# Kernel optimization log

Hardware: AMD Instinct MI355X
Metric: run time of the kernel (lower is better)

The kernel has to match this reference:

```python
import jax, jax.numpy as jnp
import numpy as np

B, C, IC, W, H, Z = 2, 128, 64, 32, 32, 128  # sub_sample=True -> new_z = Z//2
BN_EPS = 1e-5


def setup_inputs() -> dict:
    key = jax.random.key(0)
    ks = jax.random.split(key, 14)
    n = lambda k, shape, sc=1.0: jax.random.normal(k, shape, jnp.float32) * sc
    return {
        "x": n(ks[0], (B, C, W, H, Z)),
        "g_w": n(ks[1], (IC, C), 0.05), "g_b": n(ks[2], (IC,), 0.05),
        "theta_w": n(ks[3], (IC, C), 0.05), "theta_b": n(ks[4], (IC,), 0.05),
        "phi_w": n(ks[5], (IC, C), 0.05), "phi_b": n(ks[6], (IC,), 0.05),
        "cat_w": n(ks[7], (2 * IC,), 0.1),           # Conv2d(2*IC -> 1, 1x1, bias=False)
        "W_w": n(ks[8], (C, IC), 0.05), "W_b": n(ks[9], (C,), 0.05),
        "bn_g": n(ks[10], (C,), 0.1), "bn_b": n(ks[11], (C,), 0.1),
        "bn_m": n(ks[12], (C,), 0.1),
        "bn_v": jax.random.uniform(ks[13], (C,), jnp.float32, 0.5, 1.5),
    }


def _conv1x1(x, w, b):
    # 1x1x1 Conv3d == per-voxel channel matmul. x: (b,c,w,h,z), w: (o,c)
    y = jnp.einsum('bcwhz,oc->bowhz', x, w)
    return y + b[None, :, None, None, None]


def _pool_z(t):
    # MaxPool3d(kernel=(1,1,2)): halve last dim by pairwise max
    return t.reshape(*t.shape[:-1], t.shape[-1] // 2, 2).max(-1)


def reference(x, g_w, g_b, theta_w, theta_b, phi_w, phi_b, cat_w,
              W_w, W_b, bn_g, bn_b, bn_m, bn_v):
    b, c, w, h, z = x.shape
    ic = g_w.shape[0]
    nz = z // 2  # sub_sample

    g_x = _pool_z(_conv1x1(x, g_w, g_b))                     # (b, ic, w, h, nz)
    g_x = g_x.transpose(0, 2, 3, 4, 1).reshape(-1, nz, ic)    # (n, nz, ic), n=b*w*h

    theta = _conv1x1(x, theta_w, theta_b)                     # (b, ic, w, h, z)
    theta = theta.transpose(0, 2, 3, 1, 4).reshape(-1, ic, z)  # (n, ic, z)
    phi = _pool_z(_conv1x1(x, phi_w, phi_b))                  # (b, ic, w, h, nz)
    phi = phi.transpose(0, 2, 3, 1, 4).reshape(-1, ic, nz)     # (n, ic, nz)

    # concat + 1x1 Conv2d(2ic->1) + ReLU == relu(w_t . theta_i + w_p . phi_j)
    a = jnp.einsum('nci,c->ni', theta, cat_w[:ic])             # (n, z)
    bb = jnp.einsum('ncj,c->nj', phi, cat_w[ic:])              # (n, nz)
    f = jax.nn.relu(a[:, :, None] + bb[:, None, :]) / nz       # (n, z, nz), /N norm

    y = jnp.einsum('nij,njc->nic', f, g_x)                     # (n, z, ic)
    y = y.reshape(b, w, h, z, ic).transpose(0, 4, 1, 2, 3)      # (b, ic, w, h, z)

    Wy = _conv1x1(y, W_w, W_b)                                 # (b, c, w, h, z)
    scale = (bn_g / jnp.sqrt(bn_v + BN_EPS))[None, :, None, None, None]
    Wy = (Wy - bn_m[None, :, None, None, None]) * scale + bn_b[None, :, None, None, None]
    return Wy + x
```

## Files before the change

### kernel.cpp

```cpp
#include <hip/hip_runtime.h>
#include <hip/hip_bf16.h>


#define C_      128
#define IC_     64
#define Z_      128
#define NZ_     64
#define CSTRIDE 131072
#define NPIX    2048

typedef __attribute__((ext_vector_type(8))) short short8;
typedef __attribute__((ext_vector_type(4))) float f32x4;

union S8 { short8 s; uint4 u4; unsigned short h[8]; };

__device__ __forceinline__ unsigned short f2b(float f) {
    union { __hip_bfloat16 h; unsigned short u; } cv;
    cv.h = __float2bfloat16(f);
    return cv.u;
}
__device__ __forceinline__ float b2f(unsigned short u) {
    union { float f; unsigned int i; } cv; cv.i = ((unsigned int)u) << 16; return cv.f;
}

__global__ void nlb_prep(
    const float* __restrict__ g_w,   const float* __restrict__ theta_w,
    const float* __restrict__ phi_w, const float* __restrict__ W_w,
    const float* __restrict__ g_b,   const float* __restrict__ theta_b,
    const float* __restrict__ phi_b, const float* __restrict__ cat_w,
    const float* __restrict__ W_b,   const float* __restrict__ bn_g,
    const float* __restrict__ bn_b,  const float* __restrict__ bn_m,
    const float* __restrict__ bn_v,
    unsigned short* __restrict__ wcat, unsigned short* __restrict__ Wwb,
    float* __restrict__ twp, float* __restrict__ alphap, float* __restrict__ betap,
    float* __restrict__ cbp, float* __restrict__ cw2p, float* __restrict__ tbp)
{
    const int t = threadIdx.x;
    for (int idx = t; idx < 128 * 128; idx += 256) {
        const int oc = idx >> 7, c = idx & 127;
        const float v = (oc < 64) ? g_w[oc * 128 + c] : phi_w[(oc - 64) * 128 + c];
        wcat[idx] = f2b(v);
    }
    for (int idx = t; idx < 128 * 64; idx += 256)
        Wwb[idx] = f2b(W_w[idx]);
    if (t < 128) {
        float s = 0.f;
        for (int oc = 0; oc < 64; ++oc) s += cat_w[oc] * theta_w[oc * 128 + t];
        twp[t] = s;
        const float sc = bn_g[t] * rsqrtf(bn_v[t] + 1e-5f);
        alphap[t] = sc;
        betap[t]  = (W_b[t] - bn_m[t]) * sc + bn_b[t];
        cbp[t] = (t < 64) ? g_b[t] : phi_b[t - 64];
    }
    if (t < 64) cw2p[t] = cat_w[64 + t];
    if (t == 0) {
        float s = 0.f;
        for (int oc = 0; oc < 64; ++oc) s += cat_w[oc] * theta_b[oc];
        tbp[0] = s;
    }
}

__global__ __launch_bounds__(256, 3) void nlb_main(
    const float* __restrict__ x,
    const unsigned short* __restrict__ wcat,
    const unsigned short* __restrict__ Wwb,
    const float* __restrict__ twp, const float* __restrict__ alphap,
    const float* __restrict__ betap, const float* __restrict__ cbp,
    const float* __restrict__ cw2p, const float* __restrict__ tbp,
    float* __restrict__ out)
{
    const int tid  = threadIdx.x;
    const int lane = tid & 63;
    const int wv   = tid >> 6;
    const int n16  = lane & 15;
    const int q    = lane >> 4;
    const int pix  = blockIdx.x;
    const int b    = pix >> 10;
    const int wh   = pix & 1023;
    const size_t base = (size_t)b * C_ * CSTRIDE + (size_t)wh * Z_;

    __shared__ unsigned short buf1[128 * 72];
    __shared__ unsigned short xT[64 * 136];
    __shared__ unsigned short gp[64 * 72];
    __shared__ float a_s[128], b_s[64];
    __shared__ float alpha_s[128], beta_s[128], tw_s[128], cb_s[128], cw2_s[64];

    float4 ld[8];

    auto STAGE_LOAD = [&](int h) {
        #pragma unroll
        for (int it = 0; it < 8; ++it) {
            const int idx = it * 256 + tid;
            const int c = idx >> 4, zq = idx & 15;
            ld[it] = *(const float4*)&x[base + (size_t)c * CSTRIDE + h * 64 + zq * 4];
        }
    };
    auto STAGE_WRITE = [&]() {
        #pragma unroll
        for (int it = 0; it < 8; ++it) {
            const int idx = it * 256 + tid;
            const int c = idx >> 4, zq = idx & 15;
            uint2 p;
            p.x = (unsigned)f2b(ld[it].x) | ((unsigned)f2b(ld[it].y) << 16);
            p.y = (unsigned)f2b(ld[it].z) | ((unsigned)f2b(ld[it].w) << 16);
            *(uint2*)&buf1[c * 72 + zq * 4] = p;
        }
    };
    auto GATHER = [&](int h) {
        const int z = tid & 63, cb0 = (tid >> 6) * 32;
        float pa = 0.f;
        #pragma unroll
        for (int it = 0; it < 4; ++it) {
            const int c0 = cb0 + it * 8;
            unsigned short vv[8];
            #pragma unroll
            for (int u = 0; u < 8; ++u) vv[u] = buf1[(c0 + u) * 72 + z];
            #pragma unroll
            for (int u = 0; u < 8; ++u) pa += tw_s[c0 + u] * b2f(vv[u]);
            uint4 dw;
            dw.x = (unsigned)vv[0] | ((unsigned)vv[1] << 16);
            dw.y = (unsigned)vv[2] | ((unsigned)vv[3] << 16);
            dw.z = (unsigned)vv[4] | ((unsigned)vv[5] << 16);
            dw.w = (unsigned)vv[6] | ((unsigned)vv[7] << 16);
            *(uint4*)&xT[z * 136 + c0] = dw;
        }
        atomicAdd(&a_s[h * 64 + z], pa);
    };
    auto PHASEA = [&](int h) {
        short8 af[4];
        const int zl = 16 * wv + n16;
        #pragma unroll
        for (int k = 0; k < 4; ++k)
            af[k] = *(const short8*)&xT[zl * 136 + k * 32 + q * 8];
        float bsum0 = 0.f, bsum1 = 0.f;
        const int j0 = h * 32 + 8 * wv + 2 * q;
        #pragma unroll
        for (int oct = 0; oct < 8; ++oct) {
            const int oc = oct * 16 + n16;
            const float bias = cb_s[oc];
            f32x4 acc = {bias, bias, bias, bias};
            const unsigned short* wrow = wcat + oc * 128;
            #pragma unroll
            for (int k = 0; k < 4; ++k) {
                const short8 bf = *(const short8*)&wrow[k * 32 + q * 8];
                acc = __builtin_amdgcn_mfma_f32_16x16x32_bf16(af[k], bf, acc, 0, 0, 0);
            }
            const float p0 = fmaxf(acc[0], acc[1]);
            const float p1 = fmaxf(acc[2], acc[3]);
            if (oct < 4) {
                gp[oc * 72 + j0]     = f2b(p0);
                gp[oc * 72 + j0 + 1] = f2b(p1);
            } else {
                const float cw = cw2_s[oc - 64];
                bsum0 += cw * p0; bsum1 += cw * p1;
            }
        }
        #pragma unroll
        for (int m = 1; m < 16; m <<= 1) {
            bsum0 += __shfl_xor(bsum0, m);
            bsum1 += __shfl_xor(bsum1, m);
        }
        if (n16 == 0) b_s[j0]     = bsum0;
        if (n16 == 1) b_s[j0 + 1] = bsum1;
    };

    STAGE_LOAD(0);
    if (tid < 128) {
        alpha_s[tid] = alphap[tid]; beta_s[tid] = betap[tid];
        tw_s[tid] = twp[tid];       cb_s[tid] = cbp[tid];
        a_s[tid] = tbp[0];
    }
    if (tid < 64) cw2_s[tid] = cw2p[tid];
    STAGE_WRITE();
    __syncthreads();
    GATHER(0);
    __syncthreads();
    STAGE_LOAD(1);
    PHASEA(0);
    STAGE_WRITE();
    __syncthreads();
    GATHER(1);
    __syncthreads();
    PHASEA(1);
    __syncthreads();

    {
        const int i0 = 32 * wv;
        short8 bfrag[4][2];
        #pragma unroll
        for (int nt = 0; nt < 4; ++nt)
            #pragma unroll
            for (int k = 0; k < 2; ++k)
                bfrag[nt][k] = *(const short8*)&gp[(nt * 16 + n16) * 72 + k * 32 + q * 8];
        float bv[2][8];
        #pragma unroll
        for (int k = 0; k < 2; ++k)
            #pragma unroll
            for (int jj = 0; jj < 8; ++jj)
                bv[k][jj] = b_s[k * 32 + q * 8 + jj];
        f32x4 acc[2][4];
        #pragma unroll
        for (int mt = 0; mt < 2; ++mt) {
            const float ai = a_s[i0 + mt * 16 + n16];
            #pragma unroll
            for (int nt = 0; nt < 4; ++nt) acc[mt][nt] = (f32x4){0.f, 0.f, 0.f, 0.f};
            #pragma unroll
            for (int k = 0; k < 2; ++k) {
                S8 fr;
                #pragma unroll
                for (int jj = 0; jj < 8; ++jj)
                    fr.h[jj] = f2b(fmaxf(ai + bv[k][jj], 0.f) * 0.015625f);
                #pragma unroll
                for (int nt = 0; nt < 4; ++nt)
                    acc[mt][nt] = __builtin_amdgcn_mfma_f32_16x16x32_bf16(
                        fr.s, bfrag[nt][k], acc[mt][nt], 0, 0, 0);
            }
        }
        #pragma unroll
        for (int mt = 0; mt < 2; ++mt)
            #pragma unroll
            for (int nt = 0; nt < 4; ++nt)
                #pragma unroll
                for (int r = 0; r < 4; ++r) {
                    const int i  = i0 + mt * 16 + q * 4 + r;
                    const int oc = nt * 16 + n16;
                    buf1[i * 72 + oc] = f2b(acc[mt][nt][r]);
                }
    }
    __syncthreads();

    {
        const int zt0 = 2 * wv;
        short8 bC[2][2];
        #pragma unroll
        for (int zt = 0; zt < 2; ++zt)
            #pragma unroll
            for (int k = 0; k < 2; ++k) {
                const int z = (zt0 + zt) * 16 + n16;
                bC[zt][k] = *(const short8*)&buf1[z * 72 + k * 32 + q * 8];
            }
        #pragma unroll
        for (int mt = 0; mt < 8; ++mt) {
            short8 aC[2];
            const int ca = mt * 16 + n16;
            #pragma unroll
            for (int k = 0; k < 2; ++k)
                aC[k] = *(const short8*)&Wwb[ca * 64 + k * 32 + q * 8];
            float al[4], be[4];
            #pragma unroll
            for (int r = 0; r < 4; ++r) {
                const int cr = mt * 16 + q * 4 + r;
                al[r] = alpha_s[cr]; be[r] = beta_s[cr];
            }
            #pragma unroll
            for (int zt = 0; zt < 2; ++zt) {
                f32x4 acc = {0.f, 0.f, 0.f, 0.f};
                #pragma unroll
                for (int k = 0; k < 2; ++k)
                    acc = __builtin_amdgcn_mfma_f32_16x16x32_bf16(aC[k], bC[zt][k], acc, 0, 0, 0);
                const int z = (zt0 + zt) * 16 + n16;
                #pragma unroll
                for (int r = 0; r < 4; ++r) {
                    const int cr = mt * 16 + q * 4 + r;
                    const size_t gaddr = base + (size_t)cr * CSTRIDE + z;
                    out[gaddr] = acc[r] * al[r] + be[r] + x[gaddr];
                }
            }
        }
    }
}

extern "C" void kernel_launch(void* const* d_in, const int* in_sizes, int n_in,
                              void* d_out, int out_size, void* d_ws, size_t ws_size,
                              hipStream_t stream) {
    const float* x       = (const float*)d_in[0];
    const float* g_w     = (const float*)d_in[1];
    const float* g_b     = (const float*)d_in[2];
    const float* theta_w = (const float*)d_in[3];
    const float* theta_b = (const float*)d_in[4];
    const float* phi_w   = (const float*)d_in[5];
    const float* phi_b   = (const float*)d_in[6];
    const float* cat_w   = (const float*)d_in[7];
    const float* W_w     = (const float*)d_in[8];
    const float* W_b     = (const float*)d_in[9];
    const float* bn_g    = (const float*)d_in[10];
    const float* bn_b    = (const float*)d_in[11];
    const float* bn_m    = (const float*)d_in[12];
    const float* bn_v    = (const float*)d_in[13];
    float* out = (float*)d_out;

    char* ws = (char*)d_ws;
    unsigned short* wcat = (unsigned short*)ws;
    unsigned short* Wwb  = (unsigned short*)(ws + 32768);
    float* twp    = (float*)(ws + 49152);
    float* alphap = (float*)(ws + 49664);
    float* betap  = (float*)(ws + 50176);
    float* cbp    = (float*)(ws + 50688);
    float* cw2p   = (float*)(ws + 51200);
    float* tbp    = (float*)(ws + 51456);

    nlb_prep<<<dim3(1), dim3(256), 0, stream>>>(
        g_w, theta_w, phi_w, W_w, g_b, theta_b, phi_b, cat_w, W_b,
        bn_g, bn_b, bn_m, bn_v,
        wcat, Wwb, twp, alphap, betap, cbp, cw2p, tbp);

    nlb_main<<<dim3(NPIX), dim3(256), 0, stream>>>(
        x, wcat, Wwb, twp, alphap, betap, cbp, cw2p, tbp, out);
}
```

Before: 347.7 us.

## Drop xT transpose buffer, read A-fragments from staging buffer, compute theta dot via MFMA

Removes the GATHER pass and the xT transposed LDS buffer. PHASEA now builds its A fragments with strided 16-bit reads straight from buf1, and the theta projection sum is computed with an extra MFMA against a bf16 copy of the folded weights instead of scalar FMAs and LDS atomics. The buf1 row stride shrinks to 68 and the launch bounds rise to 5 blocks per CU, cutting LDS use and one sync stage to raise occupancy. The costs are scalar strided LDS reads, possible bank conflicts, a bf16-rounded theta weight, and tighter register limits.

```diff
diff --git a/kernel.cpp b/kernel.cpp
--- a/kernel.cpp
+++ b/kernel.cpp
@@ -8,11 +8,12 @@
 #define NZ_     64
 #define CSTRIDE 131072
 #define NPIX    2048
+#define BSTRIDE 68
 
 typedef __attribute__((ext_vector_type(8))) short short8;
 typedef __attribute__((ext_vector_type(4))) float f32x4;
 
-union S8 { short8 s; uint4 u4; unsigned short h[8]; };
+union S8 { short8 s; uint4 u4; uint2 u2[2]; unsigned short h[8]; };
 
 __device__ __forceinline__ unsigned short f2b(float f) {
     union { __hip_bfloat16 h; unsigned short u; } cv;
@@ -60,7 +61,7 @@
     }
 }
 
-__global__ __launch_bounds__(256, 3) void nlb_main(
+__global__ __launch_bounds__(256, 5) void nlb_main(
     const float* __restrict__ x,
     const unsigned short* __restrict__ wcat,
     const unsigned short* __restrict__ Wwb,
@@ -79,11 +80,11 @@
     const int wh   = pix & 1023;
     const size_t base = (size_t)b * C_ * CSTRIDE + (size_t)wh * Z_;
 
-    __shared__ unsigned short buf1[128 * 72];
-    __shared__ unsigned short xT[64 * 136];
+    __shared__ unsigned short buf1[128 * BSTRIDE];
     __shared__ unsigned short gp[64 * 72];
     __shared__ float a_s[128], b_s[64];
-    __shared__ float alpha_s[128], beta_s[128], tw_s[128], cb_s[128], cw2_s[64];
+    __shared__ float alpha_s[128], beta_s[128], cb_s[128], cw2_s[64];
+    __shared__ unsigned short twb_s[128];
 
     float4 ld[8];
 
@@ -103,35 +104,38 @@
             uint2 p;
             p.x = (unsigned)f2b(ld[it].x) | ((unsigned)f2b(ld[it].y) << 16);
             p.y = (unsigned)f2b(ld[it].z) | ((unsigned)f2b(ld[it].w) << 16);
-            *(uint2*)&buf1[c * 72 + zq * 4] = p;
+            *(uint2*)&buf1[c * BSTRIDE + zq * 4] = p;
         }
     };
-    auto GATHER = [&](int h) {
-        const int z = tid & 63, cb0 = (tid >> 6) * 32;
-        float pa = 0.f;
-        #pragma unroll
-        for (int it = 0; it < 4; ++it) {
-            const int c0 = cb0 + it * 8;
-            unsigned short vv[8];
-            #pragma unroll
-            for (int u = 0; u < 8; ++u) vv[u] = buf1[(c0 + u) * 72 + z];
-            #pragma unroll
-            for (int u = 0; u < 8; ++u) pa += tw_s[c0 + u] * b2f(vv[u]);
-            uint4 dw;
-            dw.x = (unsigned)vv[0] | ((unsigned)vv[1] << 16);
-            dw.y = (unsigned)vv[2] | ((unsigned)vv[3] << 16);
-            dw.z = (unsigned)vv[4] | ((unsigned)vv[5] << 16);
-            dw.w = (unsigned)vv[6] | ((unsigned)vv[7] << 16);
-            *(uint4*)&xT[z * 136 + c0] = dw;
-        }
-        atomicAdd(&a_s[h * 64 + z], pa);
-    };
+
+    const float tb = tbp[0];
+
     auto PHASEA = [&](int h) {
+        const int zl = 16 * wv + n16;
         short8 af[4];
-        const int zl = 16 * wv + n16;
-        #pragma unroll
-        for (int k = 0; k < 4; ++k)
-            af[k] = *(const short8*)&xT[zl * 136 + k * 32 + q * 8];
+        #pragma unroll
+        for (int kt = 0; kt < 4; ++kt) {
+            S8 t;
+            const int c0 = kt * 32 + q * 8;
+            #pragma unroll
+            for (int e = 0; e < 8; ++e) t.h[e] = buf1[(c0 + e) * BSTRIDE + zl];
+            af[kt] = t.s;
+        }
+        {
+            f32x4 acc = {tb, tb, tb, tb};
+            #pragma unroll
+            for (int kt = 0; kt < 4; ++kt) {
+                S8 bfa;
+                bfa.u4 = (n16 == 0) ? *(const uint4*)&twb_s[kt * 32 + q * 8]
+                                    : (uint4){0u, 0u, 0u, 0u};
+                acc = __builtin_amdgcn_mfma_f32_16x16x32_bf16(af[kt], bfa.s, acc, 0, 0, 0);
+            }
+            if (n16 == 0) {
+                #pragma unroll
+                for (int r = 0; r < 4; ++r)
+                    a_s[h * 64 + 16 * wv + q * 4 + r] = acc[r];
+            }
+        }
         float bsum0 = 0.f, bsum1 = 0.f;
         const int j0 = h * 32 + 8 * wv + 2 * q;
         #pragma unroll
@@ -167,19 +171,15 @@
     STAGE_LOAD(0);
     if (tid < 128) {
         alpha_s[tid] = alphap[tid]; beta_s[tid] = betap[tid];
-        tw_s[tid] = twp[tid];       cb_s[tid] = cbp[tid];
-        a_s[tid] = tbp[0];
+        twb_s[tid] = f2b(twp[tid]); cb_s[tid] = cbp[tid];
     }
     if (tid < 64) cw2_s[tid] = cw2p[tid];
     STAGE_WRITE();
     __syncthreads();
-    GATHER(0);
-    __syncthreads();
     STAGE_LOAD(1);
     PHASEA(0);
+    __syncthreads();
     STAGE_WRITE();
-    __syncthreads();
-    GATHER(1);
     __syncthreads();
     PHASEA(1);
     __syncthreads();
@@ -224,7 +224,7 @@
                 for (int r = 0; r < 4; ++r) {
                     const int i  = i0 + mt * 16 + q * 4 + r;
                     const int oc = nt * 16 + n16;
-                    buf1[i * 72 + oc] = f2b(acc[mt][nt][r]);
+                    buf1[i * BSTRIDE + oc] = f2b(acc[mt][nt][r]);
                 }
     }
     __syncthreads();
@@ -237,7 +237,10 @@
             #pragma unroll
             for (int k = 0; k < 2; ++k) {
                 const int z = (zt0 + zt) * 16 + n16;
-                bC[zt][k] = *(const short8*)&buf1[z * 72 + k * 32 + q * 8];
+                S8 t;
+                t.u2[0] = *(const uint2*)&buf1[z * BSTRIDE + k * 32 + q * 8];
+                t.u2[1] = *(const uint2*)&buf1[z * BSTRIDE + k * 32 + q * 8 + 4];
+                bC[zt][k] = t.s;
             }
         #pragma unroll
         for (int mt = 0; mt < 8; ++mt) {
```

Result: slower. 382.1 us (+9.9%).
